# Performance work log

Measured on AMD Instinct MI355X. Metric: run time of the kernel, lower is better.

The kernel has to match this reference:

```python
import jax, jax.numpy as jnp
import numpy as np
from jax import lax

START_IDX = 7
STOP_IDX = 8
TAGSET = 9
VOCAB = 50257
EMB = 512
HID = 1024  # bidirectional: HID//2 per direction
SEQ = 8192


def _lstm_dir(x, Wih, Whh, bih, bhh, reverse):
    # x: [T, EMB]; Wih: [4H, EMB]; Whh: [4H, H]
    H = Whh.shape[1]
    xproj = x @ Wih.T + bih  # big GEMM hoisted out of the scan: [T, 4H]

    def step(carry, xp):
        h, c = carry
        g = xp + h @ Whh.T + bhh
        i, f, gg, o = jnp.split(g, 4)
        i = jax.nn.sigmoid(i)
        f = jax.nn.sigmoid(f)
        gg = jnp.tanh(gg)
        o = jax.nn.sigmoid(o)
        c = f * c + i * gg
        h = o * jnp.tanh(c)
        return (h, c), h

    init = (jnp.zeros((H,), x.dtype), jnp.zeros((H,), x.dtype))
    _, hs = lax.scan(step, init, xproj, reverse=reverse)
    return hs  # [T, H]


def _viterbi(feats, transitions):
    # feats: [T, TAGSET]; transitions[next, prev]
    init = jnp.full((TAGSET,), -10000.0, feats.dtype).at[START_IDX].set(0.0)

    def step(fv, feat):
        scores = fv[None, :] + transitions       # [next, prev]
        bp = jnp.argmax(scores, axis=1)          # best prev per next tag
        fv_new = jnp.max(scores, axis=1) + feat
        return fv_new, bp

    fv, bptrs = lax.scan(step, init, feats)
    terminal = fv + transitions[STOP_IDX]
    best = jnp.argmax(terminal)
    path_score = terminal[best]

    def back(c, bp):
        return bp[c], c

    _, path = lax.scan(back, best, bptrs, reverse=True)  # path[t] = tag at t
    return path_score, path.astype(jnp.int32)


def setup_inputs() -> dict:
    key = jax.random.key(0)
    ks = jax.random.split(key, 13)
    H = HID // 2
    s = lambda *sh: 0.05
    inp = {
        'sentence': jax.random.randint(ks[0], (SEQ,), 0, VOCAB, dtype=jnp.int32),
        'emb': jax.random.normal(ks[1], (VOCAB + 100, EMB), jnp.float32) * 0.05,
        'Wih_f': jax.random.normal(ks[2], (4 * H, EMB), jnp.float32) * 0.05,
        'Whh_f': jax.random.normal(ks[3], (4 * H, H), jnp.float32) * 0.05,
        'bih_f': jnp.zeros((4 * H,), jnp.float32),
        'bhh_f': jnp.zeros((4 * H,), jnp.float32),
        'Wih_b': jax.random.normal(ks[4], (4 * H, EMB), jnp.float32) * 0.05,
        'Whh_b': jax.random.normal(ks[5], (4 * H, H), jnp.float32) * 0.05,
        'bih_b': jnp.zeros((4 * H,), jnp.float32),
        'bhh_b': jnp.zeros((4 * H,), jnp.float32),
        'W_out': jax.random.normal(ks[6], (TAGSET, HID), jnp.float32) * 0.05,
        'b_out': jnp.zeros((TAGSET,), jnp.float32),
    }
    trans = jax.random.normal(ks[7], (TAGSET, TAGSET), jnp.float32)
    trans = trans.at[START_IDX, :].set(-10000.0)
    trans = trans.at[:, STOP_IDX].set(-10000.0)
    inp['transitions'] = trans
    return inp


def reference(sentence, emb, Wih_f, Whh_f, bih_f, bhh_f, Wih_b, Whh_b, bih_b, bhh_b, W_out, b_out, transitions):
    x = emb[sentence]                                   # [T, EMB]
    h_f = _lstm_dir(x, Wih_f, Whh_f, bih_f, bhh_f, reverse=False)
    h_b = _lstm_dir(x, Wih_b, Whh_b, bih_b, bhh_b, reverse=True)
    lstm_out = jnp.concatenate([h_f, h_b], axis=-1)     # [T, HID]
    feats = lstm_out @ W_out.T + b_out                  # [T, TAGSET]
    score, path = _viterbi(feats, transitions)
    return score, path
```

## Files before the change

### kernel.cpp

```cpp
#include <hip/hip_runtime.h>
#include <hip/hip_bf16.h>


#define T_SEQ   8192
#define EMB     512
#define HDIM    512
#define SLICE   16
#define POISON64 0x7F7F7F7F7F7F7F7Full

__global__ __launch_bounds__(256) void gemm_xproj(
    const int* __restrict__ sentence, const float* __restrict__ emb,
    const float* __restrict__ Wih_f, const float* __restrict__ Wih_b,
    const float* __restrict__ bih_f, const float* __restrict__ bhh_f,
    const float* __restrict__ bih_b, const float* __restrict__ bhh_b,
    float* __restrict__ xprojb)
{
    __shared__ float As[16][132];
    __shared__ float Bs[16][132];
    __shared__ int   srow[128];

    const int tid = threadIdx.x;
    const int bm = blockIdx.x;
    const int bn = blockIdx.y;
    const int fwd = (bn < 16);
    const float* __restrict__ W = fwd ? Wih_f : Wih_b;
    const int jbase = bn * 128 - (fwd ? 0 : 2048);

    if (tid < 128) srow[tid] = sentence[bm * 128 + tid];
    __syncthreads();

    const int lkk = tid & 15;
    const int lr  = tid >> 4;
    int sr[8];
    #pragma unroll
    for (int i = 0; i < 8; ++i) sr[i] = srow[lr * 8 + i];
    const float* wbase = W + (size_t)(jbase + lr * 8) * EMB + lkk;

    const int tx = tid & 15, ty = tid >> 4;
    float acc[8][8] = {};

    for (int kb = 0; kb < 32; ++kb) {
        const int k0 = kb * 16;
        #pragma unroll
        for (int i = 0; i < 8; ++i) {
            As[lkk][lr * 8 + i] = emb[(size_t)sr[i] * EMB + k0 + lkk];
            Bs[lkk][lr * 8 + i] = wbase[(size_t)i * EMB + k0];
        }
        __syncthreads();
        #pragma unroll
        for (int kk = 0; kk < 16; ++kk) {
            const float4 a0 = *(const float4*)&As[kk][ty * 8];
            const float4 a1 = *(const float4*)&As[kk][ty * 8 + 4];
            const float4 b0 = *(const float4*)&Bs[kk][tx * 8];
            const float4 b1 = *(const float4*)&Bs[kk][tx * 8 + 4];
            const float av[8] = {a0.x,a0.y,a0.z,a0.w,a1.x,a1.y,a1.z,a1.w};
            const float bv[8] = {b0.x,b0.y,b0.z,b0.w,b1.x,b1.y,b1.z,b1.w};
            #pragma unroll
            for (int i = 0; i < 8; ++i)
                #pragma unroll
                for (int j = 0; j < 8; ++j)
                    acc[i][j] = fmaf(av[i], bv[j], acc[i][j]);
        }
        __syncthreads();
    }

    const float* b1p = fwd ? bih_f : bih_b;
    const float* b2p = fwd ? bhh_f : bhh_b;
    float bias[8];
    #pragma unroll
    for (int j = 0; j < 8; ++j) {
        const int jj = jbase + tx * 8 + j;
        bias[j] = b1p[jj] + b2p[jj];
    }
    #pragma unroll
    for (int i = 0; i < 8; ++i) {
        const int t = bm * 128 + ty * 8 + i;
        float4* dst = (float4*)&xprojb[(size_t)t * 4096 + bn * 128 + tx * 8];
        dst[0] = make_float4(acc[i][0] + bias[0], acc[i][1] + bias[1],
                             acc[i][2] + bias[2], acc[i][3] + bias[3]);
        dst[1] = make_float4(acc[i][4] + bias[4], acc[i][5] + bias[5],
                             acc[i][6] + bias[6], acc[i][7] + bias[7]);
    }
}

__device__ __forceinline__ float fsig(float x) { return 1.0f / (1.0f + __expf(-x)); }
__device__ __forceinline__ float ftanh(float x) {
    const float e = __expf(-2.0f * fabsf(x));
    return copysignf((1.0f - e) / (1.0f + e), x);
}
__device__ __forceinline__ unsigned long long pack2(float a, float b) {
    return (unsigned long long)__float_as_uint(a) |
           ((unsigned long long)__float_as_uint(b) << 32);
}

__global__ __launch_bounds__(320, 1) void lstm_scan(
    const float* __restrict__ xprojb,
    const float* __restrict__ Whh_f, const float* __restrict__ Whh_b,
    float* __restrict__ hseq)
{
    const int tid  = threadIdx.x;
    const int lane = tid & 63;
    const int wv   = tid >> 6;
    const int blk  = blockIdx.x;
    const int dir  = blk & 1;
    const int sub  = blk >> 1;
    const float* __restrict__ Whh = dir ? Whh_b : Whh_f;
    float* hs = hseq + (size_t)dir * T_SEQ * HDIM;

    __shared__ __align__(16) float hst[2][4][128];
    __shared__ __align__(16) float partials[2][4][64];
    __shared__ __align__(8)  float ownh[2][SLICE];
    __shared__ unsigned int cnt;
    __shared__ unsigned int ownflag;

    if (tid == 0) { cnt = 0u; ownflag = 0u; }
    __syncthreads();

    if (wv == 0) {
        float c_state = 0.0f;
        const int  m   = lane & 15;
        const bool fin = lane < 16;
        #pragma unroll 1
        for (int s = 0; s < T_SEQ; ++s) {
            const int t = dir ? (T_SEQ - 1 - s) : s;
            const int p = s & 1;
            float xp0 = 0.f, xp1 = 0.f, xp2 = 0.f, xp3 = 0.f;
            if (fin) {
                const float* xr = xprojb + (size_t)t * 4096 + dir * 2048 + sub * SLICE + m;
                xp0 = xr[0]; xp1 = xr[512]; xp2 = xr[1024]; xp3 = xr[1536];
            }
            const unsigned target = 4u * (unsigned)(s + 1);
            while (__hip_atomic_load(&cnt, __ATOMIC_ACQUIRE,
                                     __HIP_MEMORY_SCOPE_WORKGROUP) < target) {}
            float h = 0.0f;
            if (fin) {
                const float si = partials[p][0][m]      + partials[p][1][m]
                               + partials[p][2][m]      + partials[p][3][m];
                const float sf = partials[p][0][16 + m] + partials[p][1][16 + m]
                               + partials[p][2][16 + m] + partials[p][3][16 + m];
                const float sg = partials[p][0][32 + m] + partials[p][1][32 + m]
                               + partials[p][2][32 + m] + partials[p][3][32 + m];
                const float so = partials[p][0][48 + m] + partials[p][1][48 + m]
                               + partials[p][2][48 + m] + partials[p][3][48 + m];
                const float i_ = fsig(si + xp0);
                const float f_ = fsig(sf + xp1);
                const float g_ = ftanh(sg + xp2);
                const float o_ = fsig(so + xp3);
                c_state = fmaf(f_, c_state, i_ * g_);
                h = o_ * ftanh(c_state);
                ownh[p][m] = h;
            }
            if (lane == 0)
                __hip_atomic_store(&ownflag, (unsigned)(s + 1), __ATOMIC_RELEASE,
                                   __HIP_MEMORY_SCOPE_WORKGROUP);
            const float ha = __shfl(h, lane * 2);
            const float hb = __shfl(h, lane * 2 + 1);
            if (lane < 8) {
                unsigned long long* hp =
                    (unsigned long long*)(hs + (size_t)t * HDIM + sub * SLICE);
                __hip_atomic_store(hp + lane, pack2(ha, hb), __ATOMIC_RELAXED,
                                   __HIP_MEMORY_SCOPE_AGENT);
            }
        }
    } else {
        const int c  = wv - 1;
        const int rp = lane & 31;
        const int kh = lane >> 5;
        const int r0 = rp * 2;
        const int grow  = (r0 >> 4) * 512 + sub * SLICE + (r0 & 15);
        const int kbase = c * 128 + kh * 64;
        float w0[64], w1[64];
        {
            const float* src0 = Whh + (size_t)grow * 512 + kbase;
            const float* src1 = src0 + 512;
            #pragma unroll
            for (int j = 0; j < 16; ++j) {
                const float4 a = *(const float4*)(src0 + 4 * j);
                const float4 b = *(const float4*)(src1 + 4 * j);
                w0[4*j] = a.x; w0[4*j+1] = a.y; w0[4*j+2] = a.z; w0[4*j+3] = a.w;
                w1[4*j] = b.x; w1[4*j+1] = b.y; w1[4*j+2] = b.z; w1[4*j+3] = b.w;
            }
        }
        #pragma unroll
        for (int j = 0; j < 64; ++j) {
            asm volatile("" : "+v"(w0[j]));
            asm volatile("" : "+v"(w1[j]));
        }

        const bool ownlane = (c == (sub >> 3)) && ((lane >> 3) == (sub & 7));

        #pragma unroll 1
        for (int s = 0; s < T_SEQ; ++s) {
            const int t = dir ? (T_SEQ - 1 - s) : s;
            const int p = s & 1;
            float2 hv2;
            if (s == 0) {
                hv2 = make_float2(0.f, 0.f);
            } else if (ownlane) {
                while (__hip_atomic_load(&ownflag, __ATOMIC_ACQUIRE,
                                         __HIP_MEMORY_SCOPE_WORKGROUP) < (unsigned)s) {}
                const int pp = (s - 1) & 1;
                const int j  = lane & 7;
                hv2.x = ownh[pp][2 * j];
                hv2.y = ownh[pp][2 * j + 1];
            } else {
                const int tprev = dir ? (t + 1) : (t - 1);
                const unsigned long long* hp =
                    (const unsigned long long*)(hs + (size_t)tprev * HDIM) + c * 64 + lane;
                unsigned long long u = __hip_atomic_load(hp, __ATOMIC_RELAXED,
                                                         __HIP_MEMORY_SCOPE_AGENT);
                while (u == POISON64)
                    u = __hip_atomic_load(hp, __ATOMIC_RELAXED, __HIP_MEMORY_SCOPE_AGENT);
                hv2.x = __uint_as_float((unsigned)(u & 0xffffffffull));
                hv2.y = __uint_as_float((unsigned)(u >> 32));
            }
            ((float2*)&hst[p][c][0])[lane] = hv2;

            float acc0 = 0.f, acc1 = 0.f;
            const float4* hb = (const float4*)&hst[p][c][kh * 64];
            #pragma unroll
            for (int j = 0; j < 16; ++j) {
                const float4 hv = hb[j];
                acc0 = fmaf(w0[4*j],   hv.x, acc0); acc1 = fmaf(w1[4*j],   hv.x, acc1);
                acc0 = fmaf(w0[4*j+1], hv.y, acc0); acc1 = fmaf(w1[4*j+1], hv.y, acc1);
                acc0 = fmaf(w0[4*j+2], hv.z, acc0); acc1 = fmaf(w1[4*j+2], hv.z, acc1);
                acc0 = fmaf(w0[4*j+3], hv.w, acc0); acc1 = fmaf(w1[4*j+3], hv.w, acc1);
            }
            acc0 += __shfl_xor(acc0, 32);
            acc1 += __shfl_xor(acc1, 32);
            if (lane < 32)
                ((float2*)&partials[p][c][0])[lane] = make_float2(acc0, acc1);
            if (lane == 0)
                __hip_atomic_fetch_add(&cnt, 1u, __ATOMIC_RELEASE,
                                       __HIP_MEMORY_SCOPE_WORKGROUP);
        }
    }
}

__global__ __launch_bounds__(256) void feats_kernel(
    const float* __restrict__ hseq, const float* __restrict__ W_out,
    const float* __restrict__ b_out, float* __restrict__ feats)
{
    const int idx = blockIdx.x * 256 + threadIdx.x;
    if (idx >= T_SEQ * 9) return;
    const int t = idx / 9;
    const int n = idx - t * 9;
    const float4* hf = (const float4*)(hseq + (size_t)t * HDIM);
    const float4* hb = (const float4*)(hseq + (size_t)(T_SEQ + t) * HDIM);
    const float4* wf = (const float4*)(W_out + (size_t)n * 1024);
    const float4* wb = wf + 128;
    float acc = b_out[n];
    #pragma unroll 8
    for (int i = 0; i < 128; ++i) {
        const float4 a = hf[i], w = wf[i];
        acc = fmaf(a.x, w.x, acc); acc = fmaf(a.y, w.y, acc);
        acc = fmaf(a.z, w.z, acc); acc = fmaf(a.w, w.w, acc);
    }
    #pragma unroll 8
    for (int i = 0; i < 128; ++i) {
        const float4 a = hb[i], w = wb[i];
        acc = fmaf(a.x, w.x, acc); acc = fmaf(a.y, w.y, acc);
        acc = fmaf(a.z, w.z, acc); acc = fmaf(a.w, w.w, acc);
    }
    feats[idx] = acc;
}

__global__ __launch_bounds__(64) void viterbi_kernel(
    const float* __restrict__ feats, const float* __restrict__ trans,
    unsigned long long* __restrict__ bpw, float* __restrict__ out)
{
    const int lane = threadIdx.x;
    __shared__ __align__(16) float flds[1024 * 9];
    __shared__ unsigned char path_lds[T_SEQ];

    float tr[9];
    #pragma unroll
    for (int p = 0; p < 9; ++p) tr[p] = 0.f;
    float tstop = 0.f;
    if (lane < 9) {
        #pragma unroll
        for (int p = 0; p < 9; ++p) tr[p] = trans[lane * 9 + p];
        tstop = trans[8 * 9 + lane];
    }
    float fv = (lane == 7) ? 0.0f : -10000.0f;

    for (int ch = 0; ch < 8; ++ch) {
        const float4* src = (const float4*)(feats + (size_t)ch * 9216);
        #pragma unroll
        for (int i = 0; i < 36; ++i)
            ((float4*)flds)[lane + i * 64] = src[lane + i * 64];
        __syncthreads();

        for (int tt = 0; tt < 1024; ++tt) {
            const int t = ch * 1024 + tt;
            const float f0 = __shfl(fv, 0), f1 = __shfl(fv, 1), f2 = __shfl(fv, 2);
            const float f3 = __shfl(fv, 3), f4 = __shfl(fv, 4), f5 = __shfl(fv, 5);
            const float f6 = __shfl(fv, 6), f7 = __shfl(fv, 7), f8 = __shfl(fv, 8);
            const float s0 = f0 + tr[0], s1 = f1 + tr[1], s2 = f2 + tr[2];
            const float s3 = f3 + tr[3], s4 = f4 + tr[4], s5 = f5 + tr[5];
            const float s6 = f6 + tr[6], s7 = f7 + tr[7], s8 = f8 + tr[8];
            const float mx = fmaxf(fmaxf(fmaxf(fmaxf(s0, s1), fmaxf(s2, s3)),
                                         fmaxf(fmaxf(s4, s5), fmaxf(s6, s7))), s8);
            const unsigned bits =
                (s0 >= mx ? 1u : 0u)   | (s1 >= mx ? 2u : 0u)   | (s2 >= mx ? 4u : 0u) |
                (s3 >= mx ? 8u : 0u)   | (s4 >= mx ? 16u : 0u)  | (s5 >= mx ? 32u : 0u) |
                (s6 >= mx ? 64u : 0u)  | (s7 >= mx ? 128u : 0u) | (s8 >= mx ? 256u : 0u);
            const int bi = __ffs(bits) - 1;
            const float feat = (lane < 9) ? flds[tt * 9 + lane] : 0.0f;
            fv = mx + feat;
            const unsigned long long b0 = __ballot(bi & 1);
            const unsigned long long b1 = __ballot(bi & 2);
            const unsigned long long b2 = __ballot(bi & 4);
            const unsigned long long b3 = __ballot(bi & 8);
            if (lane == 0) {
                bpw[t] = (b0 & 511ull) | ((b1 & 511ull) << 9) |
                         ((b2 & 511ull) << 18) | ((b3 & 511ull) << 27);
            }
        }
        __syncthreads();
    }

    const float term = fv + tstop;
    const float t0 = __shfl(term, 0), t1 = __shfl(term, 1), t2 = __shfl(term, 2);
    const float t3 = __shfl(term, 3), t4 = __shfl(term, 4), t5 = __shfl(term, 5);
    const float t6 = __shfl(term, 6), t7 = __shfl(term, 7), t8 = __shfl(term, 8);
    const float mxt = fmaxf(fmaxf(fmaxf(fmaxf(t0, t1), fmaxf(t2, t3)),
                                  fmaxf(fmaxf(t4, t5), fmaxf(t6, t7))), t8);
    const unsigned bitst =
        (t0 >= mxt ? 1u : 0u)   | (t1 >= mxt ? 2u : 0u)   | (t2 >= mxt ? 4u : 0u) |
        (t3 >= mxt ? 8u : 0u)   | (t4 >= mxt ? 16u : 0u)  | (t5 >= mxt ? 32u : 0u) |
        (t6 >= mxt ? 64u : 0u)  | (t7 >= mxt ? 128u : 0u) | (t8 >= mxt ? 256u : 0u);
    const int best = __ffs(bitst) - 1;

    if (lane == 0) {
        out[0] = mxt;
        int c = best;
        path_lds[T_SEQ - 1] = (unsigned char)c;
        for (int thi = T_SEQ - 2; thi >= 15; thi -= 16) {
            const int tlo = thi - 15;
            unsigned long long wbuf[16];
            #pragma unroll
            for (int i = 0; i < 16; ++i) wbuf[i] = bpw[tlo + 1 + i];
            #pragma unroll
            for (int i = 15; i >= 0; --i) {
                const unsigned long long wv = wbuf[i];
                c = (int)((wv >> c) & 1ull) |
                    ((int)((wv >> (9 + c)) & 1ull) << 1) |
                    ((int)((wv >> (18 + c)) & 1ull) << 2) |
                    ((int)((wv >> (27 + c)) & 1ull) << 3);
                path_lds[tlo + i] = (unsigned char)c;
            }
        }
        for (int t2i = 14; t2i >= 0; --t2i) {
            const unsigned long long wv = bpw[t2i + 1];
            c = (int)((wv >> c) & 1ull) |
                ((int)((wv >> (9 + c)) & 1ull) << 1) |
                ((int)((wv >> (18 + c)) & 1ull) << 2) |
                ((int)((wv >> (27 + c)) & 1ull) << 3);
            path_lds[t2i] = (unsigned char)c;
        }
    }
    __syncthreads();
    #pragma unroll 4
    for (int i = 0; i < T_SEQ / 64; ++i) {
        const int t = i * 64 + lane;
        out[1 + t] = (float)path_lds[t];
    }
}

extern "C" void kernel_launch(void* const* d_in, const int* in_sizes, int n_in,
                              void* d_out, int out_size, void* d_ws, size_t ws_size,
                              hipStream_t stream)
{
    (void)in_sizes; (void)n_in; (void)out_size; (void)ws_size;

    const int*   sentence = (const int*)  d_in[0];
    const float* emb      = (const float*)d_in[1];
    const float* Wih_f    = (const float*)d_in[2];
    const float* Whh_f    = (const float*)d_in[3];
    const float* bih_f    = (const float*)d_in[4];
    const float* bhh_f    = (const float*)d_in[5];
    const float* Wih_b    = (const float*)d_in[6];
    const float* Whh_b    = (const float*)d_in[7];
    const float* bih_b    = (const float*)d_in[8];
    const float* bhh_b    = (const float*)d_in[9];
    const float* W_out    = (const float*)d_in[10];
    const float* b_out    = (const float*)d_in[11];
    const float* trans    = (const float*)d_in[12];

    float* ws      = (float*)d_ws;
    float* xprojb  = ws;
    float* hseq    = ws + (size_t)T_SEQ * 4096;
    float* feats   = hseq + (size_t)2 * T_SEQ * HDIM;
    unsigned long long* bpw = (unsigned long long*)(feats + (size_t)T_SEQ * 9);

    hipMemsetAsync(hseq, 0x7F, (size_t)2 * T_SEQ * HDIM * sizeof(float), stream);

    gemm_xproj<<<dim3(64, 32), 256, 0, stream>>>(
        sentence, emb, Wih_f, Wih_b, bih_f, bhh_f, bih_b, bhh_b, xprojb);

    lstm_scan<<<dim3(64), 320, 0, stream>>>(
        xprojb, Whh_f, Whh_b, hseq);

    feats_kernel<<<dim3((T_SEQ * 9 + 255) / 256), 256, 0, stream>>>(
        hseq, W_out, b_out, feats);

    viterbi_kernel<<<dim3(1), 64, 0, stream>>>(feats, trans, bpw, (float*)d_out);
}
```

Measured before the change: 17.00 ms.

## Restructure LSTM scan so each wave independently computes gates without intra-block barriers

Replaces the producer/consumer wave arrangement (one gate wave plus four matvec waves exchanging partial sums through LDS counters) with four self-contained waves. Each wave owns four hidden units, keeps 128 weights per lane in registers, reads the full previous hidden vector from global memory, reduces with shuffles and applies the gate nonlinearities itself. This is meant to remove the LDS atomic counter handshakes and the extra wave from the per-step critical path. In exchange every wave polls the global hidden state separately, which adds redundant global traffic, and register pressure per lane rises.

```diff
diff --git a/kernel.cpp b/kernel.cpp
--- a/kernel.cpp
+++ b/kernel.cpp
@@ -5,8 +5,9 @@
 #define T_SEQ   8192
 #define EMB     512
 #define HDIM    512
-#define SLICE   16
 #define POISON64 0x7F7F7F7F7F7F7F7Full
+
+#define ALOAD(p)  __hip_atomic_load((p), __ATOMIC_RELAXED, __HIP_MEMORY_SCOPE_AGENT)
 
 __global__ __launch_bounds__(256) void gemm_xproj(
     const int* __restrict__ sentence, const float* __restrict__ emb,
@@ -92,8 +93,14 @@
     return (unsigned long long)__float_as_uint(a) |
            ((unsigned long long)__float_as_uint(b) << 32);
 }
-
-__global__ __launch_bounds__(320, 1) void lstm_scan(
+__device__ __forceinline__ float2 unpack2(unsigned long long u) {
+    return make_float2(__uint_as_float((unsigned)(u & 0xffffffffull)),
+                       __uint_as_float((unsigned)(u >> 32)));
+}
+
+#define CH 132
+
+__global__ __launch_bounds__(256, 1) void lstm_scan(
     const float* __restrict__ xprojb,
     const float* __restrict__ Whh_f, const float* __restrict__ Whh_b,
     float* __restrict__ hseq)
@@ -107,132 +114,98 @@
     const float* __restrict__ Whh = dir ? Whh_b : Whh_f;
     float* hs = hseq + (size_t)dir * T_SEQ * HDIM;
 
-    __shared__ __align__(16) float hst[2][4][128];
-    __shared__ __align__(16) float partials[2][4][64];
-    __shared__ __align__(8)  float ownh[2][SLICE];
-    __shared__ unsigned int cnt;
-    __shared__ unsigned int ownflag;
-
-    if (tid == 0) { cnt = 0u; ownflag = 0u; }
-    __syncthreads();
-
-    if (wv == 0) {
-        float c_state = 0.0f;
-        const int  m   = lane & 15;
-        const bool fin = lane < 16;
-        #pragma unroll 1
-        for (int s = 0; s < T_SEQ; ++s) {
-            const int t = dir ? (T_SEQ - 1 - s) : s;
-            const int p = s & 1;
-            float xp0 = 0.f, xp1 = 0.f, xp2 = 0.f, xp3 = 0.f;
-            if (fin) {
-                const float* xr = xprojb + (size_t)t * 4096 + dir * 2048 + sub * SLICE + m;
-                xp0 = xr[0]; xp1 = xr[512]; xp2 = xr[1024]; xp3 = xr[1536];
-            }
-            const unsigned target = 4u * (unsigned)(s + 1);
-            while (__hip_atomic_load(&cnt, __ATOMIC_ACQUIRE,
-                                     __HIP_MEMORY_SCOPE_WORKGROUP) < target) {}
-            float h = 0.0f;
-            if (fin) {
-                const float si = partials[p][0][m]      + partials[p][1][m]
-                               + partials[p][2][m]      + partials[p][3][m];
-                const float sf = partials[p][0][16 + m] + partials[p][1][16 + m]
-                               + partials[p][2][16 + m] + partials[p][3][16 + m];
-                const float sg = partials[p][0][32 + m] + partials[p][1][32 + m]
-                               + partials[p][2][32 + m] + partials[p][3][32 + m];
-                const float so = partials[p][0][48 + m] + partials[p][1][48 + m]
-                               + partials[p][2][48 + m] + partials[p][3][48 + m];
-                const float i_ = fsig(si + xp0);
-                const float f_ = fsig(sf + xp1);
-                const float g_ = ftanh(sg + xp2);
-                const float o_ = fsig(so + xp3);
-                c_state = fmaf(f_, c_state, i_ * g_);
-                h = o_ * ftanh(c_state);
-                ownh[p][m] = h;
-            }
-            if (lane == 0)
-                __hip_atomic_store(&ownflag, (unsigned)(s + 1), __ATOMIC_RELEASE,
-                                   __HIP_MEMORY_SCOPE_WORKGROUP);
-            const float ha = __shfl(h, lane * 2);
-            const float hb = __shfl(h, lane * 2 + 1);
-            if (lane < 8) {
-                unsigned long long* hp =
-                    (unsigned long long*)(hs + (size_t)t * HDIM + sub * SLICE);
-                __hip_atomic_store(hp + lane, pack2(ha, hb), __ATOMIC_RELAXED,
-                                   __HIP_MEMORY_SCOPE_AGENT);
-            }
-        }
-    } else {
-        const int c  = wv - 1;
-        const int rp = lane & 31;
-        const int kh = lane >> 5;
-        const int r0 = rp * 2;
-        const int grow  = (r0 >> 4) * 512 + sub * SLICE + (r0 & 15);
-        const int kbase = c * 128 + kh * 64;
-        float w0[64], w1[64];
-        {
-            const float* src0 = Whh + (size_t)grow * 512 + kbase;
-            const float* src1 = src0 + 512;
-            #pragma unroll
-            for (int j = 0; j < 16; ++j) {
-                const float4 a = *(const float4*)(src0 + 4 * j);
-                const float4 b = *(const float4*)(src1 + 4 * j);
-                w0[4*j] = a.x; w0[4*j+1] = a.y; w0[4*j+2] = a.z; w0[4*j+3] = a.w;
-                w1[4*j] = b.x; w1[4*j+1] = b.y; w1[4*j+2] = b.z; w1[4*j+3] = b.w;
-            }
-        }
-        #pragma unroll
-        for (int j = 0; j < 64; ++j) {
-            asm volatile("" : "+v"(w0[j]));
-            asm volatile("" : "+v"(w1[j]));
-        }
-
-        const bool ownlane = (c == (sub >> 3)) && ((lane >> 3) == (sub & 7));
-
-        #pragma unroll 1
-        for (int s = 0; s < T_SEQ; ++s) {
-            const int t = dir ? (T_SEQ - 1 - s) : s;
-            const int p = s & 1;
-            float2 hv2;
-            if (s == 0) {
-                hv2 = make_float2(0.f, 0.f);
-            } else if (ownlane) {
-                while (__hip_atomic_load(&ownflag, __ATOMIC_ACQUIRE,
-                                         __HIP_MEMORY_SCOPE_WORKGROUP) < (unsigned)s) {}
-                const int pp = (s - 1) & 1;
-                const int j  = lane & 7;
-                hv2.x = ownh[pp][2 * j];
-                hv2.y = ownh[pp][2 * j + 1];
-            } else {
-                const int tprev = dir ? (t + 1) : (t - 1);
-                const unsigned long long* hp =
-                    (const unsigned long long*)(hs + (size_t)tprev * HDIM) + c * 64 + lane;
-                unsigned long long u = __hip_atomic_load(hp, __ATOMIC_RELAXED,
-                                                         __HIP_MEMORY_SCOPE_AGENT);
-                while (u == POISON64)
-                    u = __hip_atomic_load(hp, __ATOMIC_RELAXED, __HIP_MEMORY_SCOPE_AGENT);
-                hv2.x = __uint_as_float((unsigned)(u & 0xffffffffull));
-                hv2.y = __uint_as_float((unsigned)(u >> 32));
-            }
-            ((float2*)&hst[p][c][0])[lane] = hv2;
-
-            float acc0 = 0.f, acc1 = 0.f;
-            const float4* hb = (const float4*)&hst[p][c][kh * 64];
-            #pragma unroll
-            for (int j = 0; j < 16; ++j) {
-                const float4 hv = hb[j];
-                acc0 = fmaf(w0[4*j],   hv.x, acc0); acc1 = fmaf(w1[4*j],   hv.x, acc1);
-                acc0 = fmaf(w0[4*j+1], hv.y, acc0); acc1 = fmaf(w1[4*j+1], hv.y, acc1);
-                acc0 = fmaf(w0[4*j+2], hv.z, acc0); acc1 = fmaf(w1[4*j+2], hv.z, acc1);
-                acc0 = fmaf(w0[4*j+3], hv.w, acc0); acc1 = fmaf(w1[4*j+3], hv.w, acc1);
-            }
-            acc0 += __shfl_xor(acc0, 32);
-            acc1 += __shfl_xor(acc1, 32);
-            if (lane < 32)
-                ((float2*)&partials[p][c][0])[lane] = make_float2(acc0, acc1);
-            if (lane == 0)
-                __hip_atomic_fetch_add(&cnt, 1u, __ATOMIC_RELEASE,
-                                       __HIP_MEMORY_SCOPE_WORKGROUP);
+    const int r    = lane >> 2;
+    const int kq   = lane & 3;
+    const int gate = r >> 2;
+    const int jm   = r & 3;
+    const int mloc = wv * 4 + jm;
+    const int row  = gate * 512 + sub * 16 + mloc;
+
+    float wr[128];
+    {
+        const float* src = Whh + (size_t)row * 512 + kq * 128;
+        #pragma unroll
+        for (int i = 0; i < 32; ++i) {
+            const float4 v = *(const float4*)(src + 4 * i);
+            wr[4*i] = v.x; wr[4*i+1] = v.y; wr[4*i+2] = v.z; wr[4*i+3] = v.w;
+        }
+    }
+    #pragma unroll
+    for (int i = 0; i < 128; ++i) asm volatile("" : "+v"(wr[i]));
+
+    __shared__ __align__(16) float hst[4][4 * CH];
+    float* hbuf = hst[wv];
+
+    const int  jj = (lane >> 2) & 3;
+    const bool gl = ((lane & 3) == 0) && (lane < 16);
+    float c_state = 0.0f;
+
+    #pragma unroll 1
+    for (int s = 0; s < T_SEQ; ++s) {
+        const int t = dir ? (T_SEQ - 1 - s) : s;
+
+        float xp0 = 0.f, xp1 = 0.f, xp2 = 0.f, xp3 = 0.f;
+        if (gl) {
+            const float* xr = xprojb + (size_t)t * 4096 + dir * 2048 + sub * 16 + wv * 4 + jj;
+            xp0 = xr[0]; xp1 = xr[512]; xp2 = xr[1024]; xp3 = xr[1536];
+        }
+
+        float2 v0, v1, v2, v3;
+        if (s == 0) {
+            v0 = v1 = v2 = v3 = make_float2(0.f, 0.f);
+        } else {
+            const int tprev = dir ? (t + 1) : (t - 1);
+            const unsigned long long* hp =
+                (const unsigned long long*)(hs + (size_t)tprev * HDIM);
+            unsigned long long u0 = ALOAD(hp + lane);
+            unsigned long long u1 = ALOAD(hp + 64 + lane);
+            unsigned long long u2 = ALOAD(hp + 128 + lane);
+            unsigned long long u3 = ALOAD(hp + 192 + lane);
+            while (u0 == POISON64) u0 = ALOAD(hp + lane);
+            while (u1 == POISON64) u1 = ALOAD(hp + 64 + lane);
+            while (u2 == POISON64) u2 = ALOAD(hp + 128 + lane);
+            while (u3 == POISON64) u3 = ALOAD(hp + 192 + lane);
+            v0 = unpack2(u0); v1 = unpack2(u1); v2 = unpack2(u2); v3 = unpack2(u3);
+        }
+        *(float2*)(hbuf + 0 * CH + 2 * lane) = v0;
+        *(float2*)(hbuf + 1 * CH + 2 * lane) = v1;
+        *(float2*)(hbuf + 2 * CH + 2 * lane) = v2;
+        *(float2*)(hbuf + 3 * CH + 2 * lane) = v3;
+
+        float acc = 0.f;
+        const float4* h4 = (const float4*)(hbuf + kq * CH);
+        #pragma unroll
+        for (int i2 = 0; i2 < 32; ++i2) {
+            const float4 hv = h4[i2];
+            acc = fmaf(wr[4*i2],   hv.x, acc);
+            acc = fmaf(wr[4*i2+1], hv.y, acc);
+            acc = fmaf(wr[4*i2+2], hv.z, acc);
+            acc = fmaf(wr[4*i2+3], hv.w, acc);
+        }
+        acc += __shfl_xor(acc, 1);
+        acc += __shfl_xor(acc, 2);
+
+        const float si = __shfl(acc, jj * 4);
+        const float sf = __shfl(acc, jj * 4 + 16);
+        const float sg = __shfl(acc, jj * 4 + 32);
+        const float so = __shfl(acc, jj * 4 + 48);
+
+        float h = 0.f;
+        if (gl) {
+            const float i_ = fsig(si + xp0);
+            const float f_ = fsig(sf + xp1);
+            const float g_ = ftanh(sg + xp2);
+            const float o_ = fsig(so + xp3);
+            c_state = fmaf(f_, c_state, i_ * g_);
+            h = o_ * ftanh(c_state);
+        }
+        const float ha = __shfl(h, lane * 8);
+        const float hb = __shfl(h, lane * 8 + 4);
+        if (lane < 2) {
+            unsigned long long* hdst =
+                (unsigned long long*)(hs + (size_t)t * HDIM + sub * 16 + wv * 4);
+            __hip_atomic_store(hdst + lane, pack2(ha, hb), __ATOMIC_RELAXED,
+                               __HIP_MEMORY_SCOPE_AGENT);
         }
     }
 }
@@ -343,20 +316,20 @@
             for (int i = 0; i < 16; ++i) wbuf[i] = bpw[tlo + 1 + i];
             #pragma unroll
             for (int i = 15; i >= 0; --i) {
-                const unsigned long long wv = wbuf[i];
-                c = (int)((wv >> c) & 1ull) |
-                    ((int)((wv >> (9 + c)) & 1ull) << 1) |
-                    ((int)((wv >> (18 + c)) & 1ull) << 2) |
-                    ((int)((wv >> (27 + c)) & 1ull) << 3);
+                const unsigned long long wvv = wbuf[i];
+                c = (int)((wvv >> c) & 1ull) |
+                    ((int)((wvv >> (9 + c)) & 1ull) << 1) |
+                    ((int)((wvv >> (18 + c)) & 1ull) << 2) |
+                    ((int)((wvv >> (27 + c)) & 1ull) << 3);
                 path_lds[tlo + i] = (unsigned char)c;
             }
         }
         for (int t2i = 14; t2i >= 0; --t2i) {
-            const unsigned long long wv = bpw[t2i + 1];
-            c = (int)((wv >> c) & 1ull) |
-                ((int)((wv >> (9 + c)) & 1ull) << 1) |
-                ((int)((wv >> (18 + c)) & 1ull) << 2) |
-                ((int)((wv >> (27 + c)) & 1ull) << 3);
+            const unsigned long long wvv = bpw[t2i + 1];
+            c = (int)((wvv >> c) & 1ull) |
+                ((int)((wvv >> (9 + c)) & 1ull) << 1) |
+                ((int)((wvv >> (18 + c)) & 1ull) << 2) |
+                ((int)((wvv >> (27 + c)) & 1ull) << 3);
             path_lds[t2i] = (unsigned char)c;
         }
     }
@@ -399,7 +372,7 @@
     gemm_xproj<<<dim3(64, 32), 256, 0, stream>>>(
         sentence, emb, Wih_f, Wih_b, bih_f, bhh_f, bih_b, bhh_b, xprojb);
 
-    lstm_scan<<<dim3(64), 320, 0, stream>>>(
+    lstm_scan<<<dim3(64), 256, 0, stream>>>(
         xprojb, Whh_f, Whh_b, hseq);
 
     feats_kernel<<<dim3((T_SEQ * 9 + 255) / 256), 256, 0, stream>>>(
```

Result: slower. 24.72 ms (+45.4%).

## Fuse input-projection GEMM with LSTM scan in one persistent kernel

Applied to the files above, without the earlier changes.

Merges the xproj GEMM and the recurrent LSTM scan into a single launch. The first 32 blocks run both directions of the scan, and the remaining 2048 blocks compute GEMM tiles ordered from both ends of the sequence. The scan polls a poisoned xprojb buffer until its rows are written, so the serial recurrence can start before the GEMM finishes. The cost is an extra memset of xprojb, 640-thread blocks in which GEMM blocks idle 384 threads, and a dependence on the scan blocks being scheduled before, or concurrently with, the GEMM blocks. The asm barriers that pinned the weight registers are also removed.

```diff
diff --git a/kernel.cpp b/kernel.cpp
--- a/kernel.cpp
+++ b/kernel.cpp
@@ -7,163 +7,189 @@
 #define HDIM    512
 #define SLICE   16
 #define POISON64 0x7F7F7F7F7F7F7F7Full
-
-__global__ __launch_bounds__(256) void gemm_xproj(
+#define POISON32 0x7F7F7F7Fu
+
+#define ALOAD(p)      __hip_atomic_load((p), __ATOMIC_RELAXED, __HIP_MEMORY_SCOPE_AGENT)
+#define ASTORE(p, v)  __hip_atomic_store((p), (v), __ATOMIC_RELAXED, __HIP_MEMORY_SCOPE_AGENT)
+#define ALOAD32(p)    __hip_atomic_load((p), __ATOMIC_RELAXED, __HIP_MEMORY_SCOPE_AGENT)
+
+__device__ __forceinline__ float fsig(float x) { return 1.0f / (1.0f + __expf(-x)); }
+__device__ __forceinline__ float ftanh(float x) {
+    const float e = __expf(-2.0f * fabsf(x));
+    return copysignf((1.0f - e) / (1.0f + e), x);
+}
+__device__ __forceinline__ unsigned long long pack2(float a, float b) {
+    return (unsigned long long)__float_as_uint(a) |
+           ((unsigned long long)__float_as_uint(b) << 32);
+}
+__device__ __forceinline__ float2 unpack2(unsigned long long u) {
+    return make_float2(__uint_as_float((unsigned)(u & 0xffffffffull)),
+                       __uint_as_float((unsigned)(u >> 32)));
+}
+
+__global__ __launch_bounds__(640, 1) void fused_main(
     const int* __restrict__ sentence, const float* __restrict__ emb,
     const float* __restrict__ Wih_f, const float* __restrict__ Wih_b,
     const float* __restrict__ bih_f, const float* __restrict__ bhh_f,
     const float* __restrict__ bih_b, const float* __restrict__ bhh_b,
-    float* __restrict__ xprojb)
+    const float* __restrict__ Whh_f, const float* __restrict__ Whh_b,
+    float* __restrict__ xprojb, float* __restrict__ hseq)
 {
     __shared__ float As[16][132];
     __shared__ float Bs[16][132];
     __shared__ int   srow[128];
+    __shared__ __align__(16) float hst[2][2][4][128];
+    __shared__ __align__(16) float partials[2][2][4][64];
+    __shared__ __align__(8)  float ownh[2][2][SLICE];
+    __shared__ unsigned int cnt[2];
+    __shared__ unsigned int ownflag[2];
 
     const int tid = threadIdx.x;
-    const int bm = blockIdx.x;
-    const int bn = blockIdx.y;
-    const int fwd = (bn < 16);
-    const float* __restrict__ W = fwd ? Wih_f : Wih_b;
-    const int jbase = bn * 128 - (fwd ? 0 : 2048);
-
-    if (tid < 128) srow[tid] = sentence[bm * 128 + tid];
-    __syncthreads();
-
-    const int lkk = tid & 15;
-    const int lr  = tid >> 4;
-    int sr[8];
-    #pragma unroll
-    for (int i = 0; i < 8; ++i) sr[i] = srow[lr * 8 + i];
-    const float* wbase = W + (size_t)(jbase + lr * 8) * EMB + lkk;
-
-    const int tx = tid & 15, ty = tid >> 4;
-    float acc[8][8] = {};
-
-    for (int kb = 0; kb < 32; ++kb) {
-        const int k0 = kb * 16;
-        #pragma unroll
-        for (int i = 0; i < 8; ++i) {
-            As[lkk][lr * 8 + i] = emb[(size_t)sr[i] * EMB + k0 + lkk];
-            Bs[lkk][lr * 8 + i] = wbase[(size_t)i * EMB + k0];
-        }
+
+    if (blockIdx.x >= 32) {
+        const int bid = blockIdx.x - 32;
+        const int bmr = bid >> 5;
+        const int bn  = bid & 31;
+        const int bm  = (bmr & 1) ? (63 - (bmr >> 1)) : (bmr >> 1);
+        const int fwd = (bn < 16);
+        const float* __restrict__ W = fwd ? Wih_f : Wih_b;
+        const int jbase = bn * 128 - (fwd ? 0 : 2048);
+        const bool act = (tid < 256);
+
+        if (tid < 128) srow[tid] = sentence[bm * 128 + tid];
         __syncthreads();
-        #pragma unroll
-        for (int kk = 0; kk < 16; ++kk) {
-            const float4 a0 = *(const float4*)&As[kk][ty * 8];
-            const float4 a1 = *(const float4*)&As[kk][ty * 8 + 4];
-            const float4 b0 = *(const float4*)&Bs[kk][tx * 8];
-            const float4 b1 = *(const float4*)&Bs[kk][tx * 8 + 4];
-            const float av[8] = {a0.x,a0.y,a0.z,a0.w,a1.x,a1.y,a1.z,a1.w};
-            const float bv[8] = {b0.x,b0.y,b0.z,b0.w,b1.x,b1.y,b1.z,b1.w};
-            #pragma unroll
-            for (int i = 0; i < 8; ++i)
+
+        const int lkk = tid & 15;
+        const int lr  = (tid & 255) >> 4;
+        int sr[8];
+        float acc[8][8] = {};
+        const float* wbase = W + (size_t)(jbase + lr * 8) * EMB + lkk;
+        if (act) {
+            #pragma unroll
+            for (int i = 0; i < 8; ++i) sr[i] = srow[lr * 8 + i];
+        }
+        const int tx = tid & 15, ty = (tid & 255) >> 4;
+
+        for (int kb = 0; kb < 32; ++kb) {
+            const int k0 = kb * 16;
+            if (act) {
                 #pragma unroll
-                for (int j = 0; j < 8; ++j)
-                    acc[i][j] = fmaf(av[i], bv[j], acc[i][j]);
-        }
-        __syncthreads();
-    }
-
-    const float* b1p = fwd ? bih_f : bih_b;
-    const float* b2p = fwd ? bhh_f : bhh_b;
-    float bias[8];
-    #pragma unroll
-    for (int j = 0; j < 8; ++j) {
-        const int jj = jbase + tx * 8 + j;
-        bias[j] = b1p[jj] + b2p[jj];
-    }
-    #pragma unroll
-    for (int i = 0; i < 8; ++i) {
-        const int t = bm * 128 + ty * 8 + i;
-        float4* dst = (float4*)&xprojb[(size_t)t * 4096 + bn * 128 + tx * 8];
-        dst[0] = make_float4(acc[i][0] + bias[0], acc[i][1] + bias[1],
-                             acc[i][2] + bias[2], acc[i][3] + bias[3]);
-        dst[1] = make_float4(acc[i][4] + bias[4], acc[i][5] + bias[5],
-                             acc[i][6] + bias[6], acc[i][7] + bias[7]);
-    }
-}
-
-__device__ __forceinline__ float fsig(float x) { return 1.0f / (1.0f + __expf(-x)); }
-__device__ __forceinline__ float ftanh(float x) {
-    const float e = __expf(-2.0f * fabsf(x));
-    return copysignf((1.0f - e) / (1.0f + e), x);
-}
-__device__ __forceinline__ unsigned long long pack2(float a, float b) {
-    return (unsigned long long)__float_as_uint(a) |
-           ((unsigned long long)__float_as_uint(b) << 32);
-}
-
-__global__ __launch_bounds__(320, 1) void lstm_scan(
-    const float* __restrict__ xprojb,
-    const float* __restrict__ Whh_f, const float* __restrict__ Whh_b,
-    float* __restrict__ hseq)
-{
-    const int tid  = threadIdx.x;
-    const int lane = tid & 63;
-    const int wv   = tid >> 6;
-    const int blk  = blockIdx.x;
-    const int dir  = blk & 1;
-    const int sub  = blk >> 1;
+                for (int i = 0; i < 8; ++i) {
+                    As[lkk][lr * 8 + i] = emb[(size_t)sr[i] * EMB + k0 + lkk];
+                    Bs[lkk][lr * 8 + i] = wbase[(size_t)i * EMB + k0];
+                }
+            }
+            __syncthreads();
+            if (act) {
+                #pragma unroll
+                for (int kk = 0; kk < 16; ++kk) {
+                    const float4 a0 = *(const float4*)&As[kk][ty * 8];
+                    const float4 a1 = *(const float4*)&As[kk][ty * 8 + 4];
+                    const float4 b0 = *(const float4*)&Bs[kk][tx * 8];
+                    const float4 b1 = *(const float4*)&Bs[kk][tx * 8 + 4];
+                    const float av[8] = {a0.x,a0.y,a0.z,a0.w,a1.x,a1.y,a1.z,a1.w};
+                    const float bv[8] = {b0.x,b0.y,b0.z,b0.w,b1.x,b1.y,b1.z,b1.w};
+                    #pragma unroll
+                    for (int i = 0; i < 8; ++i)
+                        #pragma unroll
+                        for (int j = 0; j < 8; ++j)
+                            acc[i][j] = fmaf(av[i], bv[j], acc[i][j]);
+                }
+            }
+            __syncthreads();
+        }
+
+        if (act) {
+            const float* b1p = fwd ? bih_f : bih_b;
+            const float* b2p = fwd ? bhh_f : bhh_b;
+            float bias[8];
+            #pragma unroll
+            for (int j = 0; j < 8; ++j) {
+                const int jj = jbase + tx * 8 + j;
+                bias[j] = b1p[jj] + b2p[jj];
+            }
+            #pragma unroll
+            for (int i = 0; i < 8; ++i) {
+                const int t = bm * 128 + ty * 8 + i;
+                float4* dst = (float4*)&xprojb[(size_t)t * 4096 + bn * 128 + tx * 8];
+                dst[0] = make_float4(acc[i][0] + bias[0], acc[i][1] + bias[1],
+                                     acc[i][2] + bias[2], acc[i][3] + bias[3]);
+                dst[1] = make_float4(acc[i][4] + bias[4], acc[i][5] + bias[5],
+                                     acc[i][6] + bias[6], acc[i][7] + bias[7]);
+            }
+        }
+        return;
+    }
+
+    const int unit = (tid >= 320) ? 1 : 0;
+    const int ut   = tid - unit * 320;
+    const int lane = ut & 63;
+    const int wvl  = ut >> 6;
+    const int dir  = unit;
+    const int sub  = blockIdx.x;
     const float* __restrict__ Whh = dir ? Whh_b : Whh_f;
     float* hs = hseq + (size_t)dir * T_SEQ * HDIM;
 
-    __shared__ __align__(16) float hst[2][4][128];
-    __shared__ __align__(16) float partials[2][4][64];
-    __shared__ __align__(8)  float ownh[2][SLICE];
-    __shared__ unsigned int cnt;
-    __shared__ unsigned int ownflag;
-
-    if (tid == 0) { cnt = 0u; ownflag = 0u; }
+    if (tid == 0) { cnt[0] = 0u; cnt[1] = 0u; ownflag[0] = 0u; ownflag[1] = 0u; }
     __syncthreads();
 
-    if (wv == 0) {
+    if (wvl == 0) {
         float c_state = 0.0f;
         const int  m   = lane & 15;
         const bool fin = lane < 16;
+        const float* xrbase = xprojb + (size_t)dir * 2048 + sub * SLICE + m;
         #pragma unroll 1
         for (int s = 0; s < T_SEQ; ++s) {
             const int t = dir ? (T_SEQ - 1 - s) : s;
             const int p = s & 1;
             float xp0 = 0.f, xp1 = 0.f, xp2 = 0.f, xp3 = 0.f;
+            const float* xr = xrbase + (size_t)t * 4096;
             if (fin) {
-                const float* xr = xprojb + (size_t)t * 4096 + dir * 2048 + sub * SLICE + m;
                 xp0 = xr[0]; xp1 = xr[512]; xp2 = xr[1024]; xp3 = xr[1536];
             }
             const unsigned target = 4u * (unsigned)(s + 1);
-            while (__hip_atomic_load(&cnt, __ATOMIC_ACQUIRE,
+            while (__hip_atomic_load(&cnt[unit], __ATOMIC_ACQUIRE,
                                      __HIP_MEMORY_SCOPE_WORKGROUP) < target) {}
             float h = 0.0f;
             if (fin) {
-                const float si = partials[p][0][m]      + partials[p][1][m]
-                               + partials[p][2][m]      + partials[p][3][m];
-                const float sf = partials[p][0][16 + m] + partials[p][1][16 + m]
-                               + partials[p][2][16 + m] + partials[p][3][16 + m];
-                const float sg = partials[p][0][32 + m] + partials[p][1][32 + m]
-                               + partials[p][2][32 + m] + partials[p][3][32 + m];
-                const float so = partials[p][0][48 + m] + partials[p][1][48 + m]
-                               + partials[p][2][48 + m] + partials[p][3][48 + m];
+                while (__float_as_uint(xp0) == POISON32 ||
+                       __float_as_uint(xp1) == POISON32 ||
+                       __float_as_uint(xp2) == POISON32 ||
+                       __float_as_uint(xp3) == POISON32) {
+                    xp0 = __uint_as_float(ALOAD32((const unsigned*)(xr)));
+                    xp1 = __uint_as_float(ALOAD32((const unsigned*)(xr + 512)));
+                    xp2 = __uint_as_float(ALOAD32((const unsigned*)(xr + 1024)));
+                    xp3 = __uint_as_float(ALOAD32((const unsigned*)(xr + 1536)));
+                }
+                const float si = partials[unit][p][0][m]      + partials[unit][p][1][m]
+                               + partials[unit][p][2][m]      + partials[unit][p][3][m];
+                const float sf = partials[unit][p][0][16 + m] + partials[unit][p][1][16 + m]
+                               + partials[unit][p][2][16 + m] + partials[unit][p][3][16 + m];
+                const float sg = partials[unit][p][0][32 + m] + partials[unit][p][1][32 + m]
+                               + partials[unit][p][2][32 + m] + partials[unit][p][3][32 + m];
+                const float so = partials[unit][p][0][48 + m] + partials[unit][p][1][48 + m]
+                               + partials[unit][p][2][48 + m] + partials[unit][p][3][48 + m];
                 const float i_ = fsig(si + xp0);
                 const float f_ = fsig(sf + xp1);
                 const float g_ = ftanh(sg + xp2);
                 const float o_ = fsig(so + xp3);
                 c_state = fmaf(f_, c_state, i_ * g_);
                 h = o_ * ftanh(c_state);
-                ownh[p][m] = h;
+                ownh[unit][p][m] = h;
             }
             if (lane == 0)
-                __hip_atomic_store(&ownflag, (unsigned)(s + 1), __ATOMIC_RELEASE,
+                __hip_atomic_store(&ownflag[unit], (unsigned)(s + 1), __ATOMIC_RELEASE,
                                    __HIP_MEMORY_SCOPE_WORKGROUP);
             const float ha = __shfl(h, lane * 2);
             const float hb = __shfl(h, lane * 2 + 1);
             if (lane < 8) {
                 unsigned long long* hp =
                     (unsigned long long*)(hs + (size_t)t * HDIM + sub * SLICE);
-                __hip_atomic_store(hp + lane, pack2(ha, hb), __ATOMIC_RELAXED,
-                                   __HIP_MEMORY_SCOPE_AGENT);
+                ASTORE(hp + lane, pack2(ha, hb));
             }
         }
     } else {
-        const int c  = wv - 1;
+        const int c  = wvl - 1;
         const int rp = lane & 31;
         const int kh = lane >> 5;
         const int r0 = rp * 2;
@@ -181,12 +207,6 @@
                 w1[4*j] = b.x; w1[4*j+1] = b.y; w1[4*j+2] = b.z; w1[4*j+3] = b.w;
             }
         }
-        #pragma unroll
-        for (int j = 0; j < 64; ++j) {
-            asm volatile("" : "+v"(w0[j]));
-            asm volatile("" : "+v"(w1[j]));
-        }
-
         const bool ownlane = (c == (sub >> 3)) && ((lane >> 3) == (sub & 7));
 
         #pragma unroll 1
@@ -197,27 +217,24 @@
             if (s == 0) {
                 hv2 = make_float2(0.f, 0.f);
             } else if (ownlane) {
-                while (__hip_atomic_load(&ownflag, __ATOMIC_ACQUIRE,
+                while (__hip_atomic_load(&ownflag[unit], __ATOMIC_ACQUIRE,
                                          __HIP_MEMORY_SCOPE_WORKGROUP) < (unsigned)s) {}
                 const int pp = (s - 1) & 1;
                 const int j  = lane & 7;
-                hv2.x = ownh[pp][2 * j];
-                hv2.y = ownh[pp][2 * j + 1];
+                hv2.x = ownh[unit][pp][2 * j];
+                hv2.y = ownh[unit][pp][2 * j + 1];
             } else {
                 const int tprev = dir ? (t + 1) : (t - 1);
                 const unsigned long long* hp =
                     (const unsigned long long*)(hs + (size_t)tprev * HDIM) + c * 64 + lane;
-                unsigned long long u = __hip_atomic_load(hp, __ATOMIC_RELAXED,
-                                                         __HIP_MEMORY_SCOPE_AGENT);
-                while (u == POISON64)
-                    u = __hip_atomic_load(hp, __ATOMIC_RELAXED, __HIP_MEMORY_SCOPE_AGENT);
-                hv2.x = __uint_as_float((unsigned)(u & 0xffffffffull));
-                hv2.y = __uint_as_float((unsigned)(u >> 32));
-            }
-            ((float2*)&hst[p][c][0])[lane] = hv2;
+                unsigned long long u = ALOAD(hp);
+                while (u == POISON64) u = ALOAD(hp);
+                hv2 = unpack2(u);
+            }
+            ((float2*)&hst[unit][p][c][0])[lane] = hv2;
 
             float acc0 = 0.f, acc1 = 0.f;
-            const float4* hb = (const float4*)&hst[p][c][kh * 64];
+            const float4* hb = (const float4*)&hst[unit][p][c][kh * 64];
             #pragma unroll
             for (int j = 0; j < 16; ++j) {
                 const float4 hv = hb[j];
@@ -229,9 +246,9 @@
             acc0 += __shfl_xor(acc0, 32);
             acc1 += __shfl_xor(acc1, 32);
             if (lane < 32)
-                ((float2*)&partials[p][c][0])[lane] = make_float2(acc0, acc1);
+                ((float2*)&partials[unit][p][c][0])[lane] = make_float2(acc0, acc1);
             if (lane == 0)
-                __hip_atomic_fetch_add(&cnt, 1u, __ATOMIC_RELEASE,
+                __hip_atomic_fetch_add(&cnt[unit], 1u, __ATOMIC_RELEASE,
                                        __HIP_MEMORY_SCOPE_WORKGROUP);
         }
     }
@@ -343,20 +360,20 @@
             for (int i = 0; i < 16; ++i) wbuf[i] = bpw[tlo + 1 + i];
             #pragma unroll
             for (int i = 15; i >= 0; --i) {
-                const unsigned long long wv = wbuf[i];
-                c = (int)((wv >> c) & 1ull) |
-                    ((int)((wv >> (9 + c)) & 1ull) << 1) |
-                    ((int)((wv >> (18 + c)) & 1ull) << 2) |
-                    ((int)((wv >> (27 + c)) & 1ull) << 3);
+                const unsigned long long wvv = wbuf[i];
+                c = (int)((wvv >> c) & 1ull) |
+                    ((int)((wvv >> (9 + c)) & 1ull) << 1) |
+                    ((int)((wvv >> (18 + c)) & 1ull) << 2) |
+                    ((int)((wvv >> (27 + c)) & 1ull) << 3);
                 path_lds[tlo + i] = (unsigned char)c;
             }
         }
         for (int t2i = 14; t2i >= 0; --t2i) {
-            const unsigned long long wv = bpw[t2i + 1];
-            c = (int)((wv >> c) & 1ull) |
-                ((int)((wv >> (9 + c)) & 1ull) << 1) |
-                ((int)((wv >> (18 + c)) & 1ull) << 2) |
-                ((int)((wv >> (27 + c)) & 1ull) << 3);
+            const unsigned long long wvv = bpw[t2i + 1];
+            c = (int)((wvv >> c) & 1ull) |
+                ((int)((wvv >> (9 + c)) & 1ull) << 1) |
+                ((int)((wvv >> (18 + c)) & 1ull) << 2) |
+                ((int)((wvv >> (27 + c)) & 1ull) << 3);
             path_lds[t2i] = (unsigned char)c;
         }
     }
@@ -394,13 +411,12 @@
     float* feats   = hseq + (size_t)2 * T_SEQ * HDIM;
     unsigned long long* bpw = (unsigned long long*)(feats + (size_t)T_SEQ * 9);
 
-    hipMemsetAsync(hseq, 0x7F, (size_t)2 * T_SEQ * HDIM * sizeof(float), stream);
-
-    gemm_xproj<<<dim3(64, 32), 256, 0, stream>>>(
-        sentence, emb, Wih_f, Wih_b, bih_f, bhh_f, bih_b, bhh_b, xprojb);
-
-    lstm_scan<<<dim3(64), 320, 0, stream>>>(
-        xprojb, Whh_f, Whh_b, hseq);
+    hipMemsetAsync(xprojb, 0x7F, (size_t)T_SEQ * 4096 * sizeof(float), stream);
+    hipMemsetAsync(hseq,   0x7F, (size_t)2 * T_SEQ * HDIM * sizeof(float), stream);
+
+    fused_main<<<dim3(32 + 2048), 640, 0, stream>>>(
+        sentence, emb, Wih_f, Wih_b, bih_f, bhh_f, bih_b, bhh_b,
+        Whh_f, Whh_b, xprojb, hseq);
 
     feats_kernel<<<dim3((T_SEQ * 9 + 255) / 256), 256, 0, stream>>>(
         hseq, W_out, b_out, feats);
```

Result: slower. 20.00 ms (+17.7%).
